# Performance work log

Measured on AMD Instinct MI355X. Metric: run time of the kernel, lower is better.

Reference implementation:

```python
import jax, jax.numpy as jnp
import numpy as np

EPS = 1e-5
N_NODES = 100000


def setup_inputs() -> dict:
    key = jax.random.key(0)
    ks = jax.random.split(key, 24)
    N, F = N_NODES, 64
    E = 1600000
    inp = {
        "x": jax.random.normal(ks[0], (N, F), dtype=jnp.float32),
        "edge_index": jax.random.randint(ks[1], (2, E), 0, N, dtype=jnp.int64),
    }
    dims = [(F, 32), (32, 64), (64, 128), (128, 1)]
    for i, (din, dout) in enumerate(dims, start=1):
        kw, kb = jax.random.split(ks[1 + i], 2)
        scale = 1.0 / np.sqrt(din)
        inp[f"W{i}"] = jax.random.uniform(kw, (din, dout), jnp.float32, -scale, scale)
        inp[f"b{i}"] = jax.random.uniform(kb, (dout,), jnp.float32, -scale, scale)
    for i, d in enumerate([32, 64, 128], start=1):
        kg, kbe, km, kv = jax.random.split(ks[8 + i], 4)
        inp[f"g{i}"] = 1.0 + 0.1 * jax.random.normal(kg, (d,), jnp.float32)
        inp[f"be{i}"] = 0.1 * jax.random.normal(kbe, (d,), jnp.float32)
        inp[f"rm{i}"] = 0.1 * jax.random.normal(km, (d,), jnp.float32)
        inp[f"rv{i}"] = 0.5 + jax.random.uniform(kv, (d,), jnp.float32)
    return inp


def _gcn_conv(x, src, dst, norm, W, b, n):
    # GCNConv: linear transform then D^-1/2 A_hat D^-1/2 aggregation (self-loops in src/dst)
    xw = x @ W  # [N, dout]
    msg = xw[src] * norm[:, None]  # [E+N, dout] gather
    return jax.ops.segment_sum(msg, dst, num_segments=n) + b


def _bn_eval(x, g, be, rm, rv):
    return (x - rm) * jax.lax.rsqrt(rv + EPS) * g + be


def reference(x, edge_index, W1, b1, W2, b2, W3, b3, W4, b4,
              g1, be1, rm1, rv1, g2, be2, rm2, rv2, g3, be3, rm3, rv3):
    n = x.shape[0]
    loop = jnp.arange(n, dtype=edge_index.dtype)
    src = jnp.concatenate([edge_index[0], loop])
    dst = jnp.concatenate([edge_index[1], loop])
    deg = jax.ops.segment_sum(jnp.ones_like(dst, dtype=x.dtype), dst, num_segments=n)
    dinv = jnp.where(deg > 0, jax.lax.rsqrt(deg), 0.0)
    norm = dinv[src] * dinv[dst]  # shared across layers

    h = _gcn_conv(x, src, dst, norm, W1, b1, n)
    h = jax.nn.elu(_bn_eval(h, g1, be1, rm1, rv1))
    h = _gcn_conv(h, src, dst, norm, W2, b2, n)
    h = jax.nn.elu(_bn_eval(h, g2, be2, rm2, rv2))
    h = _gcn_conv(h, src, dst, norm, W3, b3, n)
    h = jax.nn.elu(_bn_eval(h, g3, be3, rm3, rv3))
    h = _gcn_conv(h, src, dst, norm, W4, b4, n)
    return jax.nn.sigmoid(jax.nn.elu(h))
```

## Files before the change

### kernel.cpp

```cpp
#include <hip/hip_runtime.h>
#include <hip/hip_fp16.h>

#define EPSF 1e-5f
#define BKT_SHIFT 9
#define BKT_NODES 512
#define TILE_E 4096

typedef _Float16 half2_t __attribute__((ext_vector_type(2)));
typedef _Float16 half4_t __attribute__((ext_vector_type(4)));
typedef _Float16 half8_t __attribute__((ext_vector_type(8)));

__device__ __forceinline__ float elu_f(float x) { return x > 0.f ? x : expm1f(x); }

__device__ __forceinline__ float fdot2f(half2_t a, half2_t b, float c) {
#if __has_builtin(__builtin_amdgcn_fdot2)
    return __builtin_amdgcn_fdot2(a, b, c, false);
#else
    return c + (float)a.x * (float)b.x + (float)a.y * (float)b.y;
#endif
}
__device__ __forceinline__ half2_t bch2(unsigned u) { return __builtin_bit_cast(half2_t, u); }
__device__ __forceinline__ half4_t bch4(uint2 u) { return __builtin_bit_cast(half4_t, u); }
__device__ __forceinline__ half8_t bch8(uint4 u) { return __builtin_bit_cast(half8_t, u); }

__device__ __forceinline__ uint2 f4_to_h4(float4 v) {
    __half2 a = __floats2half2_rn(v.x, v.y);
    __half2 b = __floats2half2_rn(v.z, v.w);
    uint2 u;
    u.x = *reinterpret_cast<unsigned*>(&a);
    u.y = *reinterpret_cast<unsigned*>(&b);
    return u;
}


__global__ __launch_bounds__(256) void k_zero(int* p, int n) {
    int i = blockIdx.x * 256 + threadIdx.x;
    if (i < n) p[i] = 0;
}

__global__ __launch_bounds__(256) void k_bhist(const int* __restrict__ dst, int* __restrict__ bkt_cnt, int E) {
    __shared__ int h[256];
    int t = threadIdx.x;
    h[t] = 0;
    __syncthreads();
    for (long e = (long)blockIdx.x * 256 + t; e < E; e += (long)gridDim.x * 256)
        atomicAdd(&h[dst[e] >> BKT_SHIFT], 1);
    __syncthreads();
    if (h[t]) atomicAdd(&bkt_cnt[t], h[t]);
}

__global__ __launch_bounds__(256) void k_bscan(const int* __restrict__ bkt_cnt, int* __restrict__ bbase,
                                               int* __restrict__ cursor) {
    __shared__ int sh[256];
    int t = threadIdx.x;
    int v = bkt_cnt[t];
    sh[t] = v;
    __syncthreads();
    for (int off = 1; off < 256; off <<= 1) {
        int add = (t >= off) ? sh[t - off] : 0;
        __syncthreads();
        sh[t] += add;
        __syncthreads();
    }
    int ex = sh[t] - v;
    bbase[t] = ex;
    cursor[t] = ex;
}

__global__ __launch_bounds__(256) void k_bpart(const int* __restrict__ src, const int* __restrict__ dst,
                                               int* __restrict__ cursor, unsigned* __restrict__ csr_tmp, int E) {
    __shared__ int hcnt[256];
    __shared__ int gbase[256];
    int t = threadIdx.x;
    long tile0 = (long)blockIdx.x * TILE_E;
    hcnt[t] = 0;
    __syncthreads();
    int d[16], s[16], rk[16];
    #pragma unroll
    for (int j = 0; j < 16; ++j) {
        long e = tile0 + j * 256 + t;
        if (e < E) {
            d[j] = dst[e];
            s[j] = src[e];
            rk[j] = atomicAdd(&hcnt[d[j] >> BKT_SHIFT], 1);
        }
    }
    __syncthreads();
    int c = hcnt[t];
    if (c) gbase[t] = atomicAdd(&cursor[t], c);
    __syncthreads();
    #pragma unroll
    for (int j = 0; j < 16; ++j) {
        long e = tile0 + j * 256 + t;
        if (e < E) {
            unsigned pk = ((unsigned)(d[j] & (BKT_NODES - 1)) << 18) | (unsigned)s[j];
            csr_tmp[gbase[d[j] >> BKT_SHIFT] + rk[j]] = pk;
        }
    }
}

__global__ __launch_bounds__(256) void k_bfine(const unsigned* __restrict__ csr_tmp, const int* __restrict__ bbase,
                                               const int* __restrict__ bkt_cnt, int* __restrict__ cnt,
                                               int* __restrict__ base, float* __restrict__ dinv,
                                               int* __restrict__ csr_s, int N) {
    __shared__ int cnt5[BKT_NODES];
    __shared__ int off5[BKT_NODES];
    __shared__ int sh[256];
    int b = blockIdx.x;
    int t = threadIdx.x;
    int d0 = b << BKT_SHIFT;
    int bb = bbase[b];
    int bc = bkt_cnt[b];
    cnt5[t] = 0;
    cnt5[t + 256] = 0;
    __syncthreads();
    for (int k = t; k < bc; k += 256) atomicAdd(&cnt5[csr_tmp[bb + k] >> 18], 1);
    __syncthreads();
    int v0 = cnt5[2 * t], v1 = cnt5[2 * t + 1];
    int p = v0 + v1;
    sh[t] = p;
    __syncthreads();
    for (int off = 1; off < 256; off <<= 1) {
        int add = (t >= off) ? sh[t - off] : 0;
        __syncthreads();
        sh[t] += add;
        __syncthreads();
    }
    int pre = sh[t] - p;
    off5[2 * t] = pre;
    off5[2 * t + 1] = pre + v0;
    #pragma unroll
    for (int j = 0; j < 2; ++j) {
        int idx = 2 * t + j;
        int i = d0 + idx;
        if (i < N) {
            int c = cnt5[idx];
            base[i] = bb + off5[idx];
            cnt[i] = c;
            dinv[i] = rsqrtf((float)(c + 1));
        }
    }
    __syncthreads();
    for (int k = t; k < bc; k += 256) {
        unsigned e = csr_tmp[bb + k];
        int pos = bb + atomicAdd(&off5[e >> 18], 1);
        csr_s[pos] = (int)(e & 0x3FFFFu);
    }
}

__global__ __launch_bounds__(256) void k_gath1(const int* __restrict__ base, const int* __restrict__ cnt,
                                               const int* __restrict__ csr_s, const float* __restrict__ dinv,
                                               const uint2* __restrict__ Xh,
                                               const float* __restrict__ b, const float* __restrict__ g,
                                               const float* __restrict__ be, const float* __restrict__ rm,
                                               const float* __restrict__ rv, uint2* __restrict__ out, int n) {
    int lane = threadIdx.x & 7, nl = threadIdx.x >> 3;
    long i = (long)blockIdx.x * 32 + nl;
    if (i >= n) return;
    int k = base[i], kend = k + cnt[i];
    float di = dinv[i];
    half4_t a0 = {0, 0, 0, 0}, a1 = a0, a2 = a0, a3 = a0;
    for (; k + 3 < kend; k += 4) {
        int s0 = csr_s[k], s1 = csr_s[k + 1], s2 = csr_s[k + 2], s3 = csr_s[k + 3];
        a0 += bch4(Xh[(long)s0 * 8 + lane]);
        a1 += bch4(Xh[(long)s1 * 8 + lane]);
        a2 += bch4(Xh[(long)s2 * 8 + lane]);
        a3 += bch4(Xh[(long)s3 * 8 + lane]);
    }
    for (; k < kend; ++k) a0 += bch4(Xh[(long)csr_s[k] * 8 + lane]);
    half4_t s4 = ((a0 + a1) + (a2 + a3)) + bch4(Xh[i * 8 + lane]);
    float4 o;
    o.x = di * (float)s4[0];
    o.y = di * (float)s4[1];
    o.z = di * (float)s4[2];
    o.w = di * (float)s4[3];
    float4 bb = reinterpret_cast<const float4*>(b)[lane];
    float4 gg = reinterpret_cast<const float4*>(g)[lane];
    float4 ee = reinterpret_cast<const float4*>(be)[lane];
    float4 mm = reinterpret_cast<const float4*>(rm)[lane];
    float4 vv = reinterpret_cast<const float4*>(rv)[lane];
    o.x = di * elu_f((o.x + bb.x - mm.x) * rsqrtf(vv.x + EPSF) * gg.x + ee.x);
    o.y = di * elu_f((o.y + bb.y - mm.y) * rsqrtf(vv.y + EPSF) * gg.y + ee.y);
    o.z = di * elu_f((o.z + bb.z - mm.z) * rsqrtf(vv.z + EPSF) * gg.z + ee.z);
    o.w = di * elu_f((o.w + bb.w - mm.w) * rsqrtf(vv.w + EPSF) * gg.w + ee.w);
    out[i * 8 + lane] = f4_to_h4(o);
}

__global__ __launch_bounds__(256) void k_gather1_final(const int* __restrict__ base, const int* __restrict__ cnt,
                                                       const int* __restrict__ csr_s,
                                                       const float* __restrict__ dinv, const float* __restrict__ y,
                                                       const float* __restrict__ b4, float* __restrict__ out, int n) {
    int i = blockIdx.x * 256 + threadIdx.x;
    if (i >= n) return;
    int k = base[i];
    int kend = k + cnt[i];
    float di = dinv[i];
    float acc = 0.f;
    for (; k < kend; ++k) acc += y[csr_s[k]];
    float v = di * (acc + y[i]) + b4[0];
    v = elu_f(v);
    out[i] = 1.f / (1.f + expf(-v));
}

template<int DIN, int DOUT>
__global__ __launch_bounds__(256, 4) void k_gemm1(const float* __restrict__ X, const float* __restrict__ W,
                                                  const float* __restrict__ dinv, uint2* __restrict__ Y, int n) {
    constexpr int TR = 4;
    constexpr int FL = DOUT / 4;
    constexpr int RG = 256 / FL;
    constexpr int BR = RG * TR;
    __shared__ float Wl[DIN * DOUT];
    for (int idx = threadIdx.x; idx < DIN * DOUT; idx += 256) Wl[idx] = W[idx];
    __syncthreads();
    const int fl = threadIdx.x % FL;
    const int rg = threadIdx.x / FL;
    const int f0 = fl * 4;
    const long r0 = (long)blockIdx.x * BR + (long)rg * TR;

    float4 z; z.x = z.y = z.z = z.w = 0.f;
    float4 acc[TR];
    #pragma unroll
    for (int r = 0; r < TR; ++r) acc[r] = z;

    #pragma unroll 2
    for (int k0 = 0; k0 < DIN; k0 += 4) {
        float4 xv[TR];
        #pragma unroll
        for (int r = 0; r < TR; ++r) {
            long row = r0 + r;
            xv[r] = (row < n) ? *reinterpret_cast<const float4*>(X + row * DIN + k0) : z;
        }
        #pragma unroll
        for (int kk = 0; kk < 4; ++kk) {
            float4 w4 = *reinterpret_cast<const float4*>(&Wl[(k0 + kk) * DOUT + f0]);
            #pragma unroll
            for (int r = 0; r < TR; ++r) {
                float xs = (kk == 0) ? xv[r].x : (kk == 1) ? xv[r].y : (kk == 2) ? xv[r].z : xv[r].w;
                acc[r].x += xs * w4.x;
                acc[r].y += xs * w4.y;
                acc[r].z += xs * w4.z;
                acc[r].w += xs * w4.w;
            }
        }
    }
    #pragma unroll
    for (int r = 0; r < TR; ++r) {
        long row = r0 + r;
        if (row >= n) continue;
        float dv = dinv[row];
        float4 v = acc[r];
        v.x *= dv; v.y *= dv; v.z *= dv; v.w *= dv;
        Y[row * FL + fl] = f4_to_h4(v);
    }
}

__global__ __launch_bounds__(256, 4) void k_fuse2(const int* __restrict__ base, const int* __restrict__ cnt,
                                                  const int* __restrict__ csr_s, const float* __restrict__ dinv,
                                                  const uint2* __restrict__ Xh,
                                                  const float* __restrict__ W, const float* __restrict__ b,
                                                  const float* __restrict__ g, const float* __restrict__ be,
                                                  const float* __restrict__ rm, const float* __restrict__ rv,
                                                  uint2* __restrict__ Y,
                                                  int n) {
    __shared__ half2_t Wl2[16 * 64];
    __shared__ __align__(16) uint2 T2[32 * 8];
    __shared__ float Dl[32];
    int t = threadIdx.x;
    for (int idx = t; idx < 16 * 64; idx += 256) {
        int p = idx >> 6, j = idx & 63;
        half2_t w;
        w.x = (_Float16)W[(2 * p) * 64 + j];
        w.y = (_Float16)W[(2 * p + 1) * 64 + j];
        Wl2[idx] = w;
    }
    int lane = t & 7, nl = t >> 3;
    long i = (long)blockIdx.x * 32 + nl;
    float4 z = {0.f, 0.f, 0.f, 0.f};
    float4 o = z;
    float di = 0.f;
    if (i < n) {
        int k = base[i], kend = k + cnt[i];
        di = dinv[i];
        half4_t a0 = {0, 0, 0, 0}, a1 = a0, a2 = a0, a3 = a0;
        for (; k + 3 < kend; k += 4) {
            int s0 = csr_s[k], s1 = csr_s[k + 1], s2 = csr_s[k + 2], s3 = csr_s[k + 3];
            a0 += bch4(Xh[(long)s0 * 8 + lane]);
            a1 += bch4(Xh[(long)s1 * 8 + lane]);
            a2 += bch4(Xh[(long)s2 * 8 + lane]);
            a3 += bch4(Xh[(long)s3 * 8 + lane]);
        }
        for (; k < kend; ++k) a0 += bch4(Xh[(long)csr_s[k] * 8 + lane]);
        half4_t s4 = ((a0 + a1) + (a2 + a3)) + bch4(Xh[i * 8 + lane]);
        o.x = di * (float)s4[0];
        o.y = di * (float)s4[1];
        o.z = di * (float)s4[2];
        o.w = di * (float)s4[3];
    }
    T2[nl * 8 + lane] = f4_to_h4(o);
    if (lane == 0) Dl[nl] = di;
    __syncthreads();

    int fl = t & 15, rg = t >> 4;
    int f0 = fl * 4;
    const uint4* T4 = reinterpret_cast<const uint4*>(T2);
    float4 acc0 = z, acc1 = z;
    #pragma unroll
    for (int c = 0; c < 4; ++c) {
        uint4 ra = T4[(rg * 2 + 0) * 4 + c];
        uint4 rb = T4[(rg * 2 + 1) * 4 + c];
        #pragma unroll
        for (int q = 0; q < 4; ++q) {
            uint4 wv = *reinterpret_cast<const uint4*>(&Wl2[(c * 4 + q) * 64 + f0]);
            half2_t w0 = bch2(wv.x), w1 = bch2(wv.y), w2 = bch2(wv.z), w3 = bch2(wv.w);
            unsigned ua = (q == 0) ? ra.x : (q == 1) ? ra.y : (q == 2) ? ra.z : ra.w;
            unsigned ub = (q == 0) ? rb.x : (q == 1) ? rb.y : (q == 2) ? rb.z : rb.w;
            half2_t xa = bch2(ua), xb = bch2(ub);
            acc0.x = fdot2f(xa, w0, acc0.x); acc0.y = fdot2f(xa, w1, acc0.y);
            acc0.z = fdot2f(xa, w2, acc0.z); acc0.w = fdot2f(xa, w3, acc0.w);
            acc1.x = fdot2f(xb, w0, acc1.x); acc1.y = fdot2f(xb, w1, acc1.y);
            acc1.z = fdot2f(xb, w2, acc1.z); acc1.w = fdot2f(xb, w3, acc1.w);
        }
    }
    float4 bias = *reinterpret_cast<const float4*>(b + f0);
    float4 gg = *reinterpret_cast<const float4*>(g + f0);
    float4 ee = *reinterpret_cast<const float4*>(be + f0);
    float4 mm = *reinterpret_cast<const float4*>(rm + f0);
    float4 vv = *reinterpret_cast<const float4*>(rv + f0);
    float4 scale, shift;
    scale.x = gg.x * rsqrtf(vv.x + EPSF); shift.x = ee.x - mm.x * scale.x;
    scale.y = gg.y * rsqrtf(vv.y + EPSF); shift.y = ee.y - mm.y * scale.y;
    scale.z = gg.z * rsqrtf(vv.z + EPSF); shift.z = ee.z - mm.z * scale.z;
    scale.w = gg.w * rsqrtf(vv.w + EPSF); shift.w = ee.w - mm.w * scale.w;
    #pragma unroll
    for (int r = 0; r < 2; ++r) {
        long row = (long)blockIdx.x * 32 + rg * 2 + r;
        if (row >= n) continue;
        float4 v = r ? acc1 : acc0;
        float dv = Dl[rg * 2 + r];
        v.x = dv * elu_f((v.x + bias.x) * scale.x + shift.x);
        v.y = dv * elu_f((v.y + bias.y) * scale.y + shift.y);
        v.z = dv * elu_f((v.z + bias.z) * scale.z + shift.z);
        v.w = dv * elu_f((v.w + bias.w) * scale.w + shift.w);
        Y[row * 16 + fl] = f4_to_h4(v);
    }
}

__global__ __launch_bounds__(256, 4) void k_fuse3(const int* __restrict__ base, const int* __restrict__ cnt,
                                                  const int* __restrict__ csr_s, const float* __restrict__ dinv,
                                                  const uint4* __restrict__ Xh,
                                                  const float* __restrict__ W, const float* __restrict__ b,
                                                  const float* __restrict__ g, const float* __restrict__ be,
                                                  const float* __restrict__ rm, const float* __restrict__ rv,
                                                  const float* __restrict__ W4,
                                                  float* __restrict__ y, int n) {
    __shared__ half2_t Wl2[32 * 128];
    __shared__ uint4 T3[32 * 8];
    __shared__ float Dl[32];
    int t = threadIdx.x;
    for (int idx = t; idx < 32 * 128; idx += 256) {
        int p = idx >> 7, j = idx & 127;
        half2_t w;
        w.x = (_Float16)W[(2 * p) * 128 + j];
        w.y = (_Float16)W[(2 * p + 1) * 128 + j];
        Wl2[idx] = w;
    }
    int lane = t & 7, nl = t >> 3;
    long i = (long)blockIdx.x * 32 + nl;
    float4 z = {0.f, 0.f, 0.f, 0.f};
    float4 oLo = z, oHi = z;
    float di = 0.f;
    if (i < n) {
        int k = base[i], kend = k + cnt[i];
        di = dinv[i];
        half8_t a0 = {0, 0, 0, 0, 0, 0, 0, 0}, a1 = a0, a2 = a0, a3 = a0;
        for (; k + 3 < kend; k += 4) {
            int s0 = csr_s[k], s1 = csr_s[k + 1], s2 = csr_s[k + 2], s3 = csr_s[k + 3];
            a0 += bch8(Xh[(long)s0 * 8 + lane]);
            a1 += bch8(Xh[(long)s1 * 8 + lane]);
            a2 += bch8(Xh[(long)s2 * 8 + lane]);
            a3 += bch8(Xh[(long)s3 * 8 + lane]);
        }
        for (; k < kend; ++k) a0 += bch8(Xh[(long)csr_s[k] * 8 + lane]);
        half8_t s8 = ((a0 + a1) + (a2 + a3)) + bch8(Xh[i * 8 + lane]);
        oLo.x = di * (float)s8[0]; oLo.y = di * (float)s8[1];
        oLo.z = di * (float)s8[2]; oLo.w = di * (float)s8[3];
        oHi.x = di * (float)s8[4]; oHi.y = di * (float)s8[5];
        oHi.z = di * (float)s8[6]; oHi.w = di * (float)s8[7];
    }
    uint2 pl = f4_to_h4(oLo), ph = f4_to_h4(oHi);
    uint4 packed; packed.x = pl.x; packed.y = pl.y; packed.z = ph.x; packed.w = ph.y;
    T3[nl * 8 + lane] = packed;
    if (lane == 0) Dl[nl] = di;
    __syncthreads();

    int fl = t & 31, rg = t >> 5;
    int f0 = fl * 4;
    float4 acc[4] = {z, z, z, z};
    #pragma unroll 2
    for (int c = 0; c < 8; ++c) {
        uint4 rowc[4];
        #pragma unroll
        for (int r = 0; r < 4; ++r) rowc[r] = T3[(rg * 4 + r) * 8 + c];
        #pragma unroll
        for (int q = 0; q < 4; ++q) {
            uint4 wv = *reinterpret_cast<const uint4*>(&Wl2[(c * 4 + q) * 128 + f0]);
            half2_t w0 = bch2(wv.x), w1 = bch2(wv.y), w2 = bch2(wv.z), w3 = bch2(wv.w);
            #pragma unroll
            for (int r = 0; r < 4; ++r) {
                unsigned xu = (q == 0) ? rowc[r].x : (q == 1) ? rowc[r].y : (q == 2) ? rowc[r].z : rowc[r].w;
                half2_t xp = bch2(xu);
                acc[r].x = fdot2f(xp, w0, acc[r].x);
                acc[r].y = fdot2f(xp, w1, acc[r].y);
                acc[r].z = fdot2f(xp, w2, acc[r].z);
                acc[r].w = fdot2f(xp, w3, acc[r].w);
            }
        }
    }
    float4 bias = *reinterpret_cast<const float4*>(b + f0);
    float4 gg = *reinterpret_cast<const float4*>(g + f0);
    float4 ee = *reinterpret_cast<const float4*>(be + f0);
    float4 mm = *reinterpret_cast<const float4*>(rm + f0);
    float4 vv = *reinterpret_cast<const float4*>(rv + f0);
    float4 w4d = *reinterpret_cast<const float4*>(W4 + f0);
    float4 scale, shift;
    scale.x = gg.x * rsqrtf(vv.x + EPSF); shift.x = ee.x - mm.x * scale.x;
    scale.y = gg.y * rsqrtf(vv.y + EPSF); shift.y = ee.y - mm.y * scale.y;
    scale.z = gg.z * rsqrtf(vv.z + EPSF); shift.z = ee.z - mm.z * scale.z;
    scale.w = gg.w * rsqrtf(vv.w + EPSF); shift.w = ee.w - mm.w * scale.w;
    #pragma unroll
    for (int r = 0; r < 4; ++r) {
        long row = (long)blockIdx.x * 32 + rg * 4 + r;
        if (row >= n) continue;
        float4 v = acc[r];
        v.x = elu_f((v.x + bias.x) * scale.x + shift.x);
        v.y = elu_f((v.y + bias.y) * scale.y + shift.y);
        v.z = elu_f((v.z + bias.z) * scale.z + shift.z);
        v.w = elu_f((v.w + bias.w) * scale.w + shift.w);
        float p = v.x * w4d.x + v.y * w4d.y + v.z * w4d.z + v.w * w4d.w;
        #pragma unroll
        for (int m = 1; m < 32; m <<= 1) p += __shfl_xor(p, m, 64);
        if (fl == 0) y[row] = Dl[rg * 4 + r] * p;
    }
}


extern "C" void kernel_launch(void* const* d_in, const int* in_sizes, int n_in,
                              void* d_out, int out_size, void* d_ws, size_t ws_size,
                              hipStream_t stream) {
    const float* x   = (const float*)d_in[0];
    const int*   edg = (const int*)d_in[1];
    const float* W1 = (const float*)d_in[2];
    const float* b1 = (const float*)d_in[3];
    const float* W2 = (const float*)d_in[4];
    const float* b2 = (const float*)d_in[5];
    const float* W3 = (const float*)d_in[6];
    const float* b3 = (const float*)d_in[7];
    const float* W4 = (const float*)d_in[8];
    const float* b4 = (const float*)d_in[9];
    const float* g1  = (const float*)d_in[10];
    const float* be1 = (const float*)d_in[11];
    const float* rm1 = (const float*)d_in[12];
    const float* rv1 = (const float*)d_in[13];
    const float* g2  = (const float*)d_in[14];
    const float* be2 = (const float*)d_in[15];
    const float* rm2 = (const float*)d_in[16];
    const float* rv2 = (const float*)d_in[17];
    const float* g3  = (const float*)d_in[18];
    const float* be3 = (const float*)d_in[19];
    const float* rm3 = (const float*)d_in[20];
    const float* rv3 = (const float*)d_in[21];
    float* out = (float*)d_out;

    const int N = in_sizes[0] / 64;
    const int E = in_sizes[1] / 2;
    const int* src = edg;
    const int* dst = edg + E;
    const int NB_BKT = (N + BKT_NODES - 1) / BKT_NODES;
    const int NTILES = (E + TILE_E - 1) / TILE_E;

    int*      bkt_cnt = (int*)d_ws;
    int*      bbase   = bkt_cnt + 256;
    int*      cursor  = bbase + 256;
    int*      cnt     = cursor + 256;
    int*      base    = cnt + N;
    float*    dinv    = (float*)(base + N);
    int*      csr_s   = (int*)(dinv + N);
    float*    featA   = (float*)(csr_s + E);
    float*    featB   = featA + (size_t)N * 64;
    unsigned* csr_tmp = (unsigned*)featA;

    auto nb = [](long total) { return (int)((total + 255) / 256); };

    k_zero<<<1, 256, 0, stream>>>(bkt_cnt, 256);
    k_bhist<<<512, 256, 0, stream>>>(dst, bkt_cnt, E);
    k_bscan<<<1, 256, 0, stream>>>(bkt_cnt, bbase, cursor);
    k_bpart<<<NTILES, 256, 0, stream>>>(src, dst, cursor, csr_tmp, E);
    k_bfine<<<NB_BKT, 256, 0, stream>>>(csr_tmp, bbase, bkt_cnt, cnt, base, dinv, csr_s, N);

    k_gemm1<64, 32><<<(N + 127) / 128, 256, 0, stream>>>(x, W1, dinv, (uint2*)featB, N);
    k_gath1<<<(N + 31) / 32, 256, 0, stream>>>(base, cnt, csr_s, dinv, (const uint2*)featB,
                                               b1, g1, be1, rm1, rv1, (uint2*)featA, N);

    k_fuse2<<<(N + 31) / 32, 256, 0, stream>>>(base, cnt, csr_s, dinv, (const uint2*)featA,
                                               W2, b2, g2, be2, rm2, rv2, (uint2*)featB, N);

    k_fuse3<<<(N + 31) / 32, 256, 0, stream>>>(base, cnt, csr_s, dinv, (const uint4*)featB,
                                               W3, b3, g3, be3, rm3, rv3, W4, featA, N);

    k_gather1_final<<<nb(N), 256, 0, stream>>>(base, cnt, csr_s, dinv, featA, b4, out, N);
}
```

Measured before the change: 339.3 us.

## Precompute fp16 weights once, double fused block size, deepen gather unrolling

Adds a small kernel that converts W2 and W3 into packed half2 layout once, so the fused layer kernels copy it into shared memory with vector loads instead of converting it per block. k_fuse2 and k_fuse3 move to 512-thread blocks of 64 nodes, which halves how often the weight tile is loaded per node. The layer-1 gather unroll goes from 4 to 8 independent accumulators, and the final scalar gather gets 4 accumulators to expose more memory-level parallelism. The larger blocks and extra accumulators raise register and LDS pressure, which may lower occupancy, and the change assumes the body code in the fused kernels still indexes correctly with the new node count per block.

```diff
diff --git a/kernel.cpp b/kernel.cpp
--- a/kernel.cpp
+++ b/kernel.cpp
@@ -148,6 +148,25 @@
     }
 }
 
+__global__ __launch_bounds__(256) void k_wconv(const float* __restrict__ W2, const float* __restrict__ W3,
+                                               unsigned* __restrict__ W2h, unsigned* __restrict__ W3h) {
+    int t = blockIdx.x * 256 + threadIdx.x;
+    if (t < 16 * 64) {
+        int p = t >> 6, j = t & 63;
+        half2_t w;
+        w.x = (_Float16)W2[(2 * p) * 64 + j];
+        w.y = (_Float16)W2[(2 * p + 1) * 64 + j];
+        W2h[t] = __builtin_bit_cast(unsigned, w);
+    }
+    if (t < 32 * 128) {
+        int p = t >> 7, j = t & 127;
+        half2_t w;
+        w.x = (_Float16)W3[(2 * p) * 128 + j];
+        w.y = (_Float16)W3[(2 * p + 1) * 128 + j];
+        W3h[t] = __builtin_bit_cast(unsigned, w);
+    }
+}
+
 __global__ __launch_bounds__(256) void k_gath1(const int* __restrict__ base, const int* __restrict__ cnt,
                                                const int* __restrict__ csr_s, const float* __restrict__ dinv,
                                                const uint2* __restrict__ Xh,
@@ -159,21 +178,31 @@
     if (i >= n) return;
     int k = base[i], kend = k + cnt[i];
     float di = dinv[i];
-    half4_t a0 = {0, 0, 0, 0}, a1 = a0, a2 = a0, a3 = a0;
-    for (; k + 3 < kend; k += 4) {
+    half4_t a0 = {0, 0, 0, 0}, a1 = a0, a2 = a0, a3 = a0, a4 = a0, a5 = a0, a6 = a0, a7 = a0;
+    for (; k + 7 < kend; k += 8) {
         int s0 = csr_s[k], s1 = csr_s[k + 1], s2 = csr_s[k + 2], s3 = csr_s[k + 3];
+        int s4 = csr_s[k + 4], s5 = csr_s[k + 5], s6 = csr_s[k + 6], s7 = csr_s[k + 7];
         a0 += bch4(Xh[(long)s0 * 8 + lane]);
         a1 += bch4(Xh[(long)s1 * 8 + lane]);
         a2 += bch4(Xh[(long)s2 * 8 + lane]);
         a3 += bch4(Xh[(long)s3 * 8 + lane]);
-    }
-    for (; k < kend; ++k) a0 += bch4(Xh[(long)csr_s[k] * 8 + lane]);
-    half4_t s4 = ((a0 + a1) + (a2 + a3)) + bch4(Xh[i * 8 + lane]);
+        a4 += bch4(Xh[(long)s4 * 8 + lane]);
+        a5 += bch4(Xh[(long)s5 * 8 + lane]);
+        a6 += bch4(Xh[(long)s6 * 8 + lane]);
+        a7 += bch4(Xh[(long)s7 * 8 + lane]);
+    }
+    for (; k + 1 < kend; k += 2) {
+        int s0 = csr_s[k], s1 = csr_s[k + 1];
+        a0 += bch4(Xh[(long)s0 * 8 + lane]);
+        a1 += bch4(Xh[(long)s1 * 8 + lane]);
+    }
+    if (k < kend) a0 += bch4(Xh[(long)csr_s[k] * 8 + lane]);
+    half4_t s4v = (((a0 + a1) + (a2 + a3)) + ((a4 + a5) + (a6 + a7))) + bch4(Xh[i * 8 + lane]);
     float4 o;
-    o.x = di * (float)s4[0];
-    o.y = di * (float)s4[1];
-    o.z = di * (float)s4[2];
-    o.w = di * (float)s4[3];
+    o.x = di * (float)s4v[0];
+    o.y = di * (float)s4v[1];
+    o.z = di * (float)s4v[2];
+    o.w = di * (float)s4v[3];
     float4 bb = reinterpret_cast<const float4*>(b)[lane];
     float4 gg = reinterpret_cast<const float4*>(g)[lane];
     float4 ee = reinterpret_cast<const float4*>(be)[lane];
@@ -195,9 +224,15 @@
     int k = base[i];
     int kend = k + cnt[i];
     float di = dinv[i];
-    float acc = 0.f;
-    for (; k < kend; ++k) acc += y[csr_s[k]];
-    float v = di * (acc + y[i]) + b4[0];
+    float a0 = 0.f, a1 = 0.f, a2 = 0.f, a3 = 0.f;
+    for (; k + 3 < kend; k += 4) {
+        a0 += y[csr_s[k]];
+        a1 += y[csr_s[k + 1]];
+        a2 += y[csr_s[k + 2]];
+        a3 += y[csr_s[k + 3]];
+    }
+    for (; k < kend; ++k) a0 += y[csr_s[k]];
+    float v = di * (((a0 + a1) + (a2 + a3)) + y[i]) + b4[0];
     v = elu_f(v);
     out[i] = 1.f / (1.f + expf(-v));
 }
@@ -254,27 +289,26 @@
     }
 }
 
-__global__ __launch_bounds__(256, 4) void k_fuse2(const int* __restrict__ base, const int* __restrict__ cnt,
+__global__ __launch_bounds__(512, 8) void k_fuse2(const int* __restrict__ base, const int* __restrict__ cnt,
                                                   const int* __restrict__ csr_s, const float* __restrict__ dinv,
                                                   const uint2* __restrict__ Xh,
-                                                  const float* __restrict__ W, const float* __restrict__ b,
+                                                  const unsigned* __restrict__ W2h,
+                                                  const float* __restrict__ b,
                                                   const float* __restrict__ g, const float* __restrict__ be,
                                                   const float* __restrict__ rm, const float* __restrict__ rv,
                                                   uint2* __restrict__ Y,
                                                   int n) {
-    __shared__ half2_t Wl2[16 * 64];
-    __shared__ __align__(16) uint2 T2[32 * 8];
-    __shared__ float Dl[32];
+    __shared__ __align__(16) half2_t Wl2[16 * 64];
+    __shared__ __align__(16) uint2 T2[64 * 8];
+    __shared__ float Dl[64];
     int t = threadIdx.x;
-    for (int idx = t; idx < 16 * 64; idx += 256) {
-        int p = idx >> 6, j = idx & 63;
-        half2_t w;
-        w.x = (_Float16)W[(2 * p) * 64 + j];
-        w.y = (_Float16)W[(2 * p + 1) * 64 + j];
-        Wl2[idx] = w;
+    {
+        const uint4* Wg = reinterpret_cast<const uint4*>(W2h);
+        uint4* Wl4 = reinterpret_cast<uint4*>(Wl2);
+        if (t < 256) Wl4[t] = Wg[t];
     }
     int lane = t & 7, nl = t >> 3;
-    long i = (long)blockIdx.x * 32 + nl;
+    long i = (long)blockIdx.x * 64 + nl;
     float4 z = {0.f, 0.f, 0.f, 0.f};
     float4 o = z;
     float di = 0.f;
@@ -333,7 +367,7 @@
     scale.w = gg.w * rsqrtf(vv.w + EPSF); shift.w = ee.w - mm.w * scale.w;
     #pragma unroll
     for (int r = 0; r < 2; ++r) {
-        long row = (long)blockIdx.x * 32 + rg * 2 + r;
+        long row = (long)blockIdx.x * 64 + rg * 2 + r;
         if (row >= n) continue;
         float4 v = r ? acc1 : acc0;
         float dv = Dl[rg * 2 + r];
@@ -345,27 +379,27 @@
     }
 }
 
-__global__ __launch_bounds__(256, 4) void k_fuse3(const int* __restrict__ base, const int* __restrict__ cnt,
+__global__ __launch_bounds__(512, 8) void k_fuse3(const int* __restrict__ base, const int* __restrict__ cnt,
                                                   const int* __restrict__ csr_s, const float* __restrict__ dinv,
                                                   const uint4* __restrict__ Xh,
-                                                  const float* __restrict__ W, const float* __restrict__ b,
+                                                  const unsigned* __restrict__ W3h,
+                                                  const float* __restrict__ b,
                                                   const float* __restrict__ g, const float* __restrict__ be,
                                                   const float* __restrict__ rm, const float* __restrict__ rv,
                                                   const float* __restrict__ W4,
                                                   float* __restrict__ y, int n) {
-    __shared__ half2_t Wl2[32 * 128];
-    __shared__ uint4 T3[32 * 8];
-    __shared__ float Dl[32];
+    __shared__ __align__(16) half2_t Wl2[32 * 128];
+    __shared__ uint4 T3[64 * 8];
+    __shared__ float Dl[64];
     int t = threadIdx.x;
-    for (int idx = t; idx < 32 * 128; idx += 256) {
-        int p = idx >> 7, j = idx & 127;
-        half2_t w;
-        w.x = (_Float16)W[(2 * p) * 128 + j];
-        w.y = (_Float16)W[(2 * p + 1) * 128 + j];
-        Wl2[idx] = w;
+    {
+        const uint4* Wg = reinterpret_cast<const uint4*>(W3h);
+        uint4* Wl4 = reinterpret_cast<uint4*>(Wl2);
+        Wl4[t] = Wg[t];
+        Wl4[t + 512] = Wg[t + 512];
     }
     int lane = t & 7, nl = t >> 3;
-    long i = (long)blockIdx.x * 32 + nl;
+    long i = (long)blockIdx.x * 64 + nl;
     float4 z = {0.f, 0.f, 0.f, 0.f};
     float4 oLo = z, oHi = z;
     float di = 0.f;
@@ -429,7 +463,7 @@
     scale.w = gg.w * rsqrtf(vv.w + EPSF); shift.w = ee.w - mm.w * scale.w;
     #pragma unroll
     for (int r = 0; r < 4; ++r) {
-        long row = (long)blockIdx.x * 32 + rg * 4 + r;
+        long row = (long)blockIdx.x * 64 + rg * 4 + r;
         if (row >= n) continue;
         float4 v = acc[r];
         v.x = elu_f((v.x + bias.x) * scale.x + shift.x);
@@ -481,7 +515,9 @@
     int*      bkt_cnt = (int*)d_ws;
     int*      bbase   = bkt_cnt + 256;
     int*      cursor  = bbase + 256;
-    int*      cnt     = cursor + 256;
+    unsigned* W2h     = (unsigned*)(cursor + 256);
+    unsigned* W3h     = W2h + 1024;
+    int*      cnt     = (int*)(W3h + 4096);
     int*      base    = cnt + N;
     float*    dinv    = (float*)(base + N);
     int*      csr_s   = (int*)(dinv + N);
@@ -493,6 +529,7 @@
 
     k_zero<<<1, 256, 0, stream>>>(bkt_cnt, 256);
     k_bhist<<<512, 256, 0, stream>>>(dst, bkt_cnt, E);
+    k_wconv<<<16, 256, 0, stream>>>(W2, W3, W2h, W3h);
     k_bscan<<<1, 256, 0, stream>>>(bkt_cnt, bbase, cursor);
     k_bpart<<<NTILES, 256, 0, stream>>>(src, dst, cursor, csr_tmp, E);
     k_bfine<<<NB_BKT, 256, 0, stream>>>(csr_tmp, bbase, bkt_cnt, cnt, base, dinv, csr_s, N);
@@ -501,11 +538,11 @@
     k_gath1<<<(N + 31) / 32, 256, 0, stream>>>(base, cnt, csr_s, dinv, (const uint2*)featB,
                                                b1, g1, be1, rm1, rv1, (uint2*)featA, N);
 
-    k_fuse2<<<(N + 31) / 32, 256, 0, stream>>>(base, cnt, csr_s, dinv, (const uint2*)featA,
-                                               W2, b2, g2, be2, rm2, rv2, (uint2*)featB, N);
-
-    k_fuse3<<<(N + 31) / 32, 256, 0, stream>>>(base, cnt, csr_s, dinv, (const uint4*)featB,
-                                               W3, b3, g3, be3, rm3, rv3, W4, featA, N);
+    k_fuse2<<<(N + 63) / 64, 512, 0, stream>>>(base, cnt, csr_s, dinv, (const uint2*)featA,
+                                               W2h, b2, g2, be2, rm2, rv2, (uint2*)featB, N);
+
+    k_fuse3<<<(N + 63) / 64, 512, 0, stream>>>(base, cnt, csr_s, dinv, (const uint4*)featB,
+                                               W3h, b3, g3, be3, rm3, rv3, W4, featA, N);
 
     k_gather1_final<<<nb(N), 256, 0, stream>>>(base, cnt, csr_s, dinv, featA, b4, out, N);
 }
```

Result: slower. 557.3 us (+64.2%).
